# Optimization experiments

Hardware: AMD Instinct MI355X
Metric: run time of the kernel (lower is better)

The kernel has to match this reference:

```python
import jax, jax.numpy as jnp
import numpy as np

N_NODES = 50000
N_EDGES = 600000
NUM_FEATURES = 128
HIDDEN = 128
NUM_CLASSES = 64
NUM_GRAPHS = 128


def setup_inputs() -> dict:
    key = jax.random.key(0)
    ks = jax.random.split(key, 10)
    x = jax.random.normal(ks[0], (N_NODES, NUM_FEATURES), dtype=jnp.float32)
    edge_index = jax.random.randint(ks[1], (2, N_EDGES), 0, N_NODES, dtype=jnp.int64)
    batch = jnp.sort(jax.random.randint(ks[2], (N_NODES,), 0, NUM_GRAPHS, dtype=jnp.int64))
    def glorot(k, fan_in, fan_out):
        s = jnp.sqrt(6.0 / (fan_in + fan_out)).astype(jnp.float32)
        return jax.random.uniform(k, (fan_in, fan_out), jnp.float32, -s, s)
    W0 = glorot(ks[3], NUM_FEATURES, HIDDEN)
    b0 = jnp.zeros((HIDDEN,), jnp.float32)
    W1 = glorot(ks[4], HIDDEN, HIDDEN)
    b1 = jnp.zeros((HIDDEN,), jnp.float32)
    W2 = glorot(ks[5], HIDDEN, NUM_CLASSES)
    b2 = jnp.zeros((NUM_CLASSES,), jnp.float32)
    return {"x": x, "edge_index": edge_index, "batch": batch,
            "W0": W0, "b0": b0, "W1": W1, "b1": b1, "W2": W2, "b2": b2}


def _gcn_norm(edge_index, n_nodes):
    # add self loops, compute symmetric normalization coeffs (PyG GCNConv)
    loops = jnp.arange(n_nodes, dtype=edge_index.dtype)
    src = jnp.concatenate([edge_index[0], loops])
    dst = jnp.concatenate([edge_index[1], loops])
    deg = jax.ops.segment_sum(jnp.ones_like(dst, dtype=jnp.float32), dst,
                              num_segments=n_nodes)
    dinv = jnp.where(deg > 0, jax.lax.rsqrt(deg), 0.0)
    norm = dinv[src] * dinv[dst]  # [E + N]
    return src, dst, norm


def _gcn_conv(x, src, dst, norm, W, b, n_nodes):
    h = x @ W                                   # [N, out]
    msg = h[src] * norm[:, None]                # gather + scale per edge
    out = jax.ops.segment_sum(msg, dst, num_segments=n_nodes)  # scatter-add
    return out + b


def reference(x, edge_index, batch, W0, b0, W1, b1, W2, b2):
    n = x.shape[0]
    src, dst, norm = _gcn_norm(edge_index, n)
    h = jax.nn.relu(_gcn_conv(x, src, dst, norm, W0, b0, n))
    # F.dropout(training=self.training) is identity in eval mode
    h = jax.nn.relu(_gcn_conv(h, src, dst, norm, W1, b1, n))
    h = _gcn_conv(h, src, dst, norm, W2, b2, n)
    # global_mean_pool over batch vector
    sums = jax.ops.segment_sum(h, batch, num_segments=NUM_GRAPHS)
    cnts = jax.ops.segment_sum(jnp.ones((n,), jnp.float32), batch,
                               num_segments=NUM_GRAPHS)
    pooled = sums / jnp.maximum(cnts, 1.0)[:, None]  # [G, num_classes]
    return jax.nn.softmax(pooled, axis=1)
```

## Files before the change

kernel.cpp:

```cpp
#include <hip/hip_runtime.h>
#include <cstdint>
#include <cstddef>

typedef unsigned int uint32;


__global__ __launch_bounds__(256) void count_kernel(const int* __restrict__ dst,
                                                    int* __restrict__ counts, int e) {
  int i = blockIdx.x * 256 + threadIdx.x;
  if (i < e) atomicAdd(&counts[dst[i]], 1);
}

__global__ __launch_bounds__(256) void dinv_kernel(const int* __restrict__ counts,
                                                   float* __restrict__ dinv, int n) {
  int i = blockIdx.x * 256 + threadIdx.x;
  if (i < n) dinv[i] = rsqrtf((float)(counts[i] + 1));
}

__global__ __launch_bounds__(256) void scan1_kernel(const int* __restrict__ counts,
                                                    int* __restrict__ bsum, int n) {
  __shared__ int lds[256];
  int tid = threadIdx.x;
  int i = blockIdx.x * 256 + tid;
  lds[tid] = (i < n) ? counts[i] : 0;
  __syncthreads();
  for (int off = 128; off > 0; off >>= 1) {
    if (tid < off) lds[tid] += lds[tid + off];
    __syncthreads();
  }
  if (tid == 0) bsum[blockIdx.x] = lds[0];
}

__global__ __launch_bounds__(256) void scan2_kernel(int* __restrict__ bsum, int nb) {
  __shared__ int lds[256];
  int tid = threadIdx.x;
  int v = (tid < nb) ? bsum[tid] : 0;
  lds[tid] = v;
  __syncthreads();
  for (int off = 1; off < 256; off <<= 1) {
    int t = (tid >= off) ? lds[tid - off] : 0;
    __syncthreads();
    lds[tid] += t;
    __syncthreads();
  }
  if (tid < nb) bsum[tid] = lds[tid] - v;
}

__global__ __launch_bounds__(256) void scan3_kernel(const int* __restrict__ counts,
                                                    const int* __restrict__ bsum,
                                                    int* __restrict__ offsets, int n) {
  __shared__ int lds[256];
  int tid = threadIdx.x;
  int i = blockIdx.x * 256 + tid;
  int v = (i < n) ? counts[i] : 0;
  lds[tid] = v;
  __syncthreads();
  for (int off = 1; off < 256; off <<= 1) {
    int t = (tid >= off) ? lds[tid - off] : 0;
    __syncthreads();
    lds[tid] += t;
    __syncthreads();
  }
  if (i < n) offsets[i] = bsum[blockIdx.x] + lds[tid] - v;
}

__global__ __launch_bounds__(256) void scatter_kernel(const int* __restrict__ src,
                                                      const int* __restrict__ dst,
                                                      const float* __restrict__ dinv,
                                                      int* __restrict__ offsets,
                                                      int2* __restrict__ csr_sw, int e) {
  int i = blockIdx.x * 256 + threadIdx.x;
  if (i < e) {
    int d = dst[i], s = src[i];
    int pos = atomicAdd(&offsets[d], 1);
    csr_sw[pos] = make_int2(s, __float_as_int(dinv[s] * dinv[d]));
  }
}

__device__ __forceinline__ uint32 bf16pair(float a, float b) {
  uint32 ua = __float_as_uint(a);
  uint32 ub = __float_as_uint(b);
  ua += 0x7fffu + ((ua >> 16) & 1u);
  ub += 0x7fffu + ((ub >> 16) & 1u);
  return (ua >> 16) | (ub & 0xffff0000u);
}


template <int BM, int BN>
__global__ __launch_bounds__(256) void gemm_kernel(const float* __restrict__ X,
                                                   const float* __restrict__ W,
                                                   uint32* __restrict__ T, int M) {
  constexpr int K = 128;
  static_assert(BM * BN == 4096, "4x4 tile x 256 threads");
  __shared__ float xs[K][BM];
  __shared__ float ws[K][BN];

  int tid = threadIdx.x;
  int row0 = blockIdx.x * BM;

  {
    constexpr int TPR = 256 / BM;
    int r = tid / TPR;
    int lw = tid % TPR;
    int grow = row0 + r;
    if (grow >= M) grow = M - 1;
    const float* xp = &X[(size_t)grow * K];
#pragma unroll
    for (int u = 0; u < K / (4 * TPR); ++u) {
      int k = (lw + u * TPR) * 4;
      float4 v = *(const float4*)&xp[k];
      xs[k + 0][r] = v.x;
      xs[k + 1][r] = v.y;
      xs[k + 2][r] = v.z;
      xs[k + 3][r] = v.w;
    }
  }
  {
    const float4* wsrc = (const float4*)W;
    float4* wdst = (float4*)&ws[0][0];
#pragma unroll
    for (int u = 0; u < (K * BN) / 1024; ++u)
      wdst[tid + u * 256] = wsrc[tid + u * 256];
  }
  __syncthreads();

  int r0 = (tid % (BM / 4)) * 4;
  int c0 = (tid / (BM / 4)) * 4;
  float acc[4][4];
#pragma unroll
  for (int i = 0; i < 4; ++i)
#pragma unroll
    for (int j = 0; j < 4; ++j) acc[i][j] = 0.f;

#pragma unroll 8
  for (int k = 0; k < K; ++k) {
    float4 a = *(const float4*)&xs[k][r0];
    float4 b = *(const float4*)&ws[k][c0];
    float av[4] = {a.x, a.y, a.z, a.w};
    float bv[4] = {b.x, b.y, b.z, b.w};
#pragma unroll
    for (int i = 0; i < 4; ++i)
#pragma unroll
      for (int j = 0; j < 4; ++j) acc[i][j] += av[i] * bv[j];
  }

#pragma unroll
  for (int i = 0; i < 4; ++i) {
    int grow = row0 + r0 + i;
    if (grow < M) {
      uint2 o;
      o.x = bf16pair(acc[i][0], acc[i][1]);
      o.y = bf16pair(acc[i][2], acc[i][3]);
      *(uint2*)&T[((size_t)grow * BN + c0) >> 1] = o;
    }
  }
}


template <int F, bool RELU>
__global__ __launch_bounds__(256) void agg_kernel(const uint32* __restrict__ T,
                                                  const int2* __restrict__ csr_sw,
                                                  const int* __restrict__ offsets,
                                                  const int* __restrict__ counts,
                                                  const float* __restrict__ dinv,
                                                  const float* __restrict__ bias,
                                                  float* __restrict__ O, int n) {
  constexpr int LPN = F / 8;
  constexpr int NPB = 256 / LPN;
  constexpr int RS = F / 8;
  int tid = threadIdx.x;
  int lane = tid % LPN;
  int v = blockIdx.x * NPB + tid / LPN;
  if (v >= n) return;

  const uint4* Tv = (const uint4*)T;

#define LO(u) __uint_as_float((u) << 16)
#define HI(u) __uint_as_float((u) & 0xffff0000u)

  float dv = dinv[v];
  float sw = dv * dv;
  float a0, a1, a2, a3, a4, a5, a6, a7;
  {
    uint4 q = Tv[(size_t)v * RS + lane];
    a0 = sw * LO(q.x); a1 = sw * HI(q.x);
    a2 = sw * LO(q.y); a3 = sw * HI(q.y);
    a4 = sw * LO(q.z); a5 = sw * HI(q.z);
    a6 = sw * LO(q.w); a7 = sw * HI(q.w);
  }

  int end = offsets[v];
  int i = end - counts[v];
  for (; i + 4 <= end; i += 4) {
    int2 p0 = csr_sw[i + 0];
    int2 p1 = csr_sw[i + 1];
    int2 p2 = csr_sw[i + 2];
    int2 p3 = csr_sw[i + 3];
    uint4 u0 = Tv[(size_t)p0.x * RS + lane];
    uint4 u1 = Tv[(size_t)p1.x * RS + lane];
    uint4 u2 = Tv[(size_t)p2.x * RS + lane];
    uint4 u3 = Tv[(size_t)p3.x * RS + lane];
    float w0 = __int_as_float(p0.y), w1 = __int_as_float(p1.y);
    float w2 = __int_as_float(p2.y), w3 = __int_as_float(p3.y);
    a0 += w0 * LO(u0.x); a1 += w0 * HI(u0.x); a2 += w0 * LO(u0.y); a3 += w0 * HI(u0.y);
    a4 += w0 * LO(u0.z); a5 += w0 * HI(u0.z); a6 += w0 * LO(u0.w); a7 += w0 * HI(u0.w);
    a0 += w1 * LO(u1.x); a1 += w1 * HI(u1.x); a2 += w1 * LO(u1.y); a3 += w1 * HI(u1.y);
    a4 += w1 * LO(u1.z); a5 += w1 * HI(u1.z); a6 += w1 * LO(u1.w); a7 += w1 * HI(u1.w);
    a0 += w2 * LO(u2.x); a1 += w2 * HI(u2.x); a2 += w2 * LO(u2.y); a3 += w2 * HI(u2.y);
    a4 += w2 * LO(u2.z); a5 += w2 * HI(u2.z); a6 += w2 * LO(u2.w); a7 += w2 * HI(u2.w);
    a0 += w3 * LO(u3.x); a1 += w3 * HI(u3.x); a2 += w3 * LO(u3.y); a3 += w3 * HI(u3.y);
    a4 += w3 * LO(u3.z); a5 += w3 * HI(u3.z); a6 += w3 * LO(u3.w); a7 += w3 * HI(u3.w);
  }
  for (; i < end; ++i) {
    int2 p = csr_sw[i];
    float w = __int_as_float(p.y);
    uint4 u = Tv[(size_t)p.x * RS + lane];
    a0 += w * LO(u.x); a1 += w * HI(u.x); a2 += w * LO(u.y); a3 += w * HI(u.y);
    a4 += w * LO(u.z); a5 += w * HI(u.z); a6 += w * LO(u.w); a7 += w * HI(u.w);
  }
#undef LO
#undef HI

  int fo = lane * 8;
  float4 b0 = *(const float4*)&bias[fo];
  float4 b1 = *(const float4*)&bias[fo + 4];
  a0 += b0.x; a1 += b0.y; a2 += b0.z; a3 += b0.w;
  a4 += b1.x; a5 += b1.y; a6 += b1.z; a7 += b1.w;
  if (RELU) {
    a0 = fmaxf(a0, 0.f); a1 = fmaxf(a1, 0.f); a2 = fmaxf(a2, 0.f); a3 = fmaxf(a3, 0.f);
    a4 = fmaxf(a4, 0.f); a5 = fmaxf(a5, 0.f); a6 = fmaxf(a6, 0.f); a7 = fmaxf(a7, 0.f);
  }
  float4 o0 = {a0, a1, a2, a3};
  float4 o1 = {a4, a5, a6, a7};
  *(float4*)&O[(size_t)v * F + fo] = o0;
  *(float4*)&O[(size_t)v * F + fo + 4] = o1;
}


__global__ __launch_bounds__(256) void pool_kernel(const float* __restrict__ h3,
                                                   const int* __restrict__ batch,
                                                   float* __restrict__ pooled,
                                                   float* __restrict__ gcnt, int n) {
  constexpr int NPW = 64;
  int lane = threadIdx.x & 63;
  int wave = threadIdx.x >> 6;
  int v0 = (blockIdx.x * 4 + wave) * NPW;
  if (v0 >= n) return;
  int vend = min(v0 + NPW, n);

  float acc = 0.f;
  int cnt = 0;
  int bcur = batch[v0];
  for (int v = v0; v < vend; ++v) {
    int b = batch[v];
    if (b != bcur) {
      atomicAdd(&pooled[bcur * 64 + lane], acc);
      if (lane == 0) atomicAdd(&gcnt[bcur], (float)cnt);
      acc = 0.f; cnt = 0; bcur = b;
    }
    acc += h3[(size_t)v * 64 + lane];
    ++cnt;
  }
  atomicAdd(&pooled[bcur * 64 + lane], acc);
  if (lane == 0) atomicAdd(&gcnt[bcur], (float)cnt);
}

__global__ __launch_bounds__(64) void softmax_kernel(const float* __restrict__ pooled,
                                                     const float* __restrict__ gcnt,
                                                     float* __restrict__ out) {
  int g = blockIdx.x;
  int lane = threadIdx.x;
  float c = fmaxf(gcnt[g], 1.0f);
  float v = pooled[g * 64 + lane] / c;
  float m = v;
#pragma unroll
  for (int off = 32; off >= 1; off >>= 1) m = fmaxf(m, __shfl_xor(m, off));
  float e = expf(v - m);
  float s = e;
#pragma unroll
  for (int off = 32; off >= 1; off >>= 1) s += __shfl_xor(s, off);
  out[g * 64 + lane] = e / s;
}


extern "C" void kernel_launch(void* const* d_in, const int* in_sizes, int n_in,
                              void* d_out, int out_size, void* d_ws, size_t ws_size,
                              hipStream_t stream) {
  const float* x  = (const float*)d_in[0];
  const int* edge = (const int*)d_in[1];
  const int* batch = (const int*)d_in[2];
  const float* W0 = (const float*)d_in[3];
  const float* b0 = (const float*)d_in[4];
  const float* W1 = (const float*)d_in[5];
  const float* b1 = (const float*)d_in[6];
  const float* W2 = (const float*)d_in[7];
  const float* b2 = (const float*)d_in[8];
  float* out = (float*)d_out;

  const int N = in_sizes[2];
  const int E = in_sizes[1] / 2;
  const int* esrc = edge;
  const int* edst = edge + E;

  char* p = (char*)d_ws;
  auto alloc = [&](size_t bytes) {
    char* r = p;
    p += (bytes + 255) & ~(size_t)255;
    return r;
  };
  int*    counts  = (int*)alloc((size_t)N * 4);
  int*    offsets = (int*)alloc((size_t)N * 4);
  float*  dinv    = (float*)alloc((size_t)N * 4);
  int*    bsum    = (int*)alloc(256 * 4);
  int2*   csr_sw  = (int2*)alloc((size_t)E * 8);
  uint32* Tb      = (uint32*)alloc((size_t)N * 128 * 2);
  float*  A       = (float*)alloc((size_t)N * 128 * 4);
  float*  pooled  = (float*)alloc(128 * 64 * 4);
  float*  gcnt    = (float*)alloc(128 * 4);

  int nbN = (N + 255) / 256;
  int nbE = (E + 255) / 256;

  hipMemsetAsync(counts, 0, (size_t)N * 4, stream);
  hipMemsetAsync(pooled, 0, 128 * 64 * 4, stream);
  hipMemsetAsync(gcnt, 0, 128 * 4, stream);

  count_kernel<<<nbE, 256, 0, stream>>>(edst, counts, E);
  dinv_kernel<<<nbN, 256, 0, stream>>>(counts, dinv, N);
  scan1_kernel<<<nbN, 256, 0, stream>>>(counts, bsum, N);
  scan2_kernel<<<1, 256, 0, stream>>>(bsum, nbN);
  scan3_kernel<<<nbN, 256, 0, stream>>>(counts, bsum, offsets, N);
  scatter_kernel<<<nbE, 256, 0, stream>>>(esrc, edst, dinv, offsets, csr_sw, E);

  gemm_kernel<32, 128><<<(N + 31) / 32, 256, 0, stream>>>(x, W0, Tb, N);
  agg_kernel<128, true><<<(N + 15) / 16, 256, 0, stream>>>(Tb, csr_sw, offsets,
                                                           counts, dinv, b0, A, N);
  gemm_kernel<32, 128><<<(N + 31) / 32, 256, 0, stream>>>(A, W1, Tb, N);
  agg_kernel<128, true><<<(N + 15) / 16, 256, 0, stream>>>(Tb, csr_sw, offsets,
                                                           counts, dinv, b1, A, N);
  gemm_kernel<64, 64><<<(N + 63) / 64, 256, 0, stream>>>(A, W2, Tb, N);
  agg_kernel<64, false><<<(N + 31) / 32, 256, 0, stream>>>(Tb, csr_sw, offsets,
                                                           counts, dinv, b2, A, N);

  pool_kernel<<<(N + 255) / 256, 256, 0, stream>>>(A, batch, pooled, gcnt, N);
  softmax_kernel<<<128, 64, 0, stream>>>(pooled, gcnt, out);
}
```

Before: 335.7 us.

## Switch dense GEMMs to bf16 MFMA with swizzled LDS and pretransposed weights

Replaces the fp32 FMA GEMM with a bf16 MFMA 16x16x32 kernel. Activations are converted to bf16 while being staged into XOR-swizzled shared memory, and a new prep kernel transposes and packs the weights into bf16. The aim is to move the dense transforms onto matrix cores and shrink LDS traffic. The cost is bf16 rounding of inputs and weights, which lowers GEMM precision, plus one extra small kernel launch.

```diff
diff --git a/kernel.cpp b/kernel.cpp
--- a/kernel.cpp
+++ b/kernel.cpp
@@ -3,6 +3,9 @@
 #include <cstddef>
 
 typedef unsigned int uint32;
+typedef unsigned short uint16;
+using short8 = __attribute__((ext_vector_type(8))) short;
+using f32x4 = __attribute__((ext_vector_type(4))) float;
 
 
 __global__ __launch_bounds__(256) void count_kernel(const int* __restrict__ dst,
@@ -77,81 +80,101 @@
   }
 }
 
+__device__ __forceinline__ uint32 bf16of(float a) {
+  uint32 u = __float_as_uint(a);
+  u += 0x7fffu + ((u >> 16) & 1u);
+  return u >> 16;
+}
 __device__ __forceinline__ uint32 bf16pair(float a, float b) {
-  uint32 ua = __float_as_uint(a);
-  uint32 ub = __float_as_uint(b);
-  ua += 0x7fffu + ((ua >> 16) & 1u);
-  ub += 0x7fffu + ((ub >> 16) & 1u);
-  return (ua >> 16) | (ub & 0xffff0000u);
-}
-
-
-template <int BM, int BN>
+  return bf16of(a) | (bf16of(b) << 16);
+}
+
+__global__ __launch_bounds__(256) void wprep_kernel(const float* __restrict__ W0,
+                                                    const float* __restrict__ W1,
+                                                    const float* __restrict__ W2,
+                                                    uint32* __restrict__ Wt0,
+                                                    uint32* __restrict__ Wt1,
+                                                    uint32* __restrict__ Wt2) {
+  int b = blockIdx.x;
+  const float* W; uint32* Wt; int N; int base;
+  if (b < 32)      { W = W0; Wt = Wt0; N = 128; base = b; }
+  else if (b < 64) { W = W1; Wt = Wt1; N = 128; base = b - 32; }
+  else             { W = W2; Wt = Wt2; N = 64;  base = b - 64; }
+  int id = base * 256 + threadIdx.x;
+  int col = id % N;
+  int kp = id / N;
+  if (kp >= 64) return;
+  int k = kp * 2;
+  Wt[col * 64 + kp] = bf16pair(W[(size_t)k * N + col], W[(size_t)(k + 1) * N + col]);
+}
+
+
+template <int BN>
 __global__ __launch_bounds__(256) void gemm_kernel(const float* __restrict__ X,
-                                                   const float* __restrict__ W,
-                                                   uint32* __restrict__ T, int M) {
-  constexpr int K = 128;
-  static_assert(BM * BN == 4096, "4x4 tile x 256 threads");
-  __shared__ float xs[K][BM];
-  __shared__ float ws[K][BN];
+                                                   const uint32* __restrict__ Wt,
+                                                   uint16* __restrict__ T, int M) {
+  constexpr int K = 128, BM = 64;
+  constexpr int NT = BN / 16;
+  __shared__ alignas(16) uint16 xs[BM * K];
+  __shared__ alignas(16) uint16 wsT[BN * K];
 
   int tid = threadIdx.x;
   int row0 = blockIdx.x * BM;
 
   {
-    constexpr int TPR = 256 / BM;
-    int r = tid / TPR;
-    int lw = tid % TPR;
+    int r = tid >> 2, k0 = (tid & 3) * 32;
     int grow = row0 + r;
     if (grow >= M) grow = M - 1;
     const float* xp = &X[(size_t)grow * K];
 #pragma unroll
-    for (int u = 0; u < K / (4 * TPR); ++u) {
-      int k = (lw + u * TPR) * 4;
+    for (int u = 0; u < 8; ++u) {
+      int k = k0 + u * 4;
       float4 v = *(const float4*)&xp[k];
-      xs[k + 0][r] = v.x;
-      xs[k + 1][r] = v.y;
-      xs[k + 2][r] = v.z;
-      xs[k + 3][r] = v.w;
+      uint2 pk = make_uint2(bf16pair(v.x, v.y), bf16pair(v.z, v.w));
+      int byte = (r * 256 + k * 2) ^ ((r & 7) << 4);
+      *(uint2*)((char*)xs + byte) = pk;
     }
   }
   {
-    const float4* wsrc = (const float4*)W;
-    float4* wdst = (float4*)&ws[0][0];
-#pragma unroll
-    for (int u = 0; u < (K * BN) / 1024; ++u)
-      wdst[tid + u * 256] = wsrc[tid + u * 256];
+#pragma unroll
+    for (int u = 0; u < NT; ++u) {
+      int idx = tid + u * 256;
+      int col = idx >> 4;
+      int kb = (idx & 15) << 4;
+      uint4 v = *(const uint4*)((const char*)Wt + col * 256 + kb);
+      int byte = (col * 256 + kb) ^ ((col & 7) << 4);
+      *(uint4*)((char*)wsT + byte) = v;
+    }
   }
   __syncthreads();
 
-  int r0 = (tid % (BM / 4)) * 4;
-  int c0 = (tid / (BM / 4)) * 4;
-  float acc[4][4];
-#pragma unroll
-  for (int i = 0; i < 4; ++i)
-#pragma unroll
-    for (int j = 0; j < 4; ++j) acc[i][j] = 0.f;
-
-#pragma unroll 8
-  for (int k = 0; k < K; ++k) {
-    float4 a = *(const float4*)&xs[k][r0];
-    float4 b = *(const float4*)&ws[k][c0];
-    float av[4] = {a.x, a.y, a.z, a.w};
-    float bv[4] = {b.x, b.y, b.z, b.w};
-#pragma unroll
-    for (int i = 0; i < 4; ++i)
-#pragma unroll
-      for (int j = 0; j < 4; ++j) acc[i][j] += av[i] * bv[j];
-  }
-
-#pragma unroll
-  for (int i = 0; i < 4; ++i) {
-    int grow = row0 + r0 + i;
-    if (grow < M) {
-      uint2 o;
-      o.x = bf16pair(acc[i][0], acc[i][1]);
-      o.y = bf16pair(acc[i][2], acc[i][3]);
-      *(uint2*)&T[((size_t)grow * BN + c0) >> 1] = o;
+  int w = tid >> 6, l = tid & 63;
+  int lrow = l & 15, lk = l >> 4;
+
+  f32x4 acc[NT];
+#pragma unroll
+  for (int n = 0; n < NT; ++n) acc[n] = {0.f, 0.f, 0.f, 0.f};
+
+#pragma unroll
+  for (int c = 0; c < 4; ++c) {
+    int ak = c * 32 + lk * 8;
+    int ar = w * 16 + lrow;
+    short8 afrag = *(const short8*)((const char*)xs + ((ar * 256 + ak * 2) ^ ((ar & 7) << 4)));
+#pragma unroll
+    for (int n = 0; n < NT; ++n) {
+      int bc = n * 16 + lrow;
+      short8 bfrag = *(const short8*)((const char*)wsT + ((bc * 256 + ak * 2) ^ ((bc & 7) << 4)));
+      acc[n] = __builtin_amdgcn_mfma_f32_16x16x32_bf16(afrag, bfrag, acc[n], 0, 0, 0);
+    }
+  }
+
+#pragma unroll
+  for (int n = 0; n < NT; ++n) {
+#pragma unroll
+    for (int r = 0; r < 4; ++r) {
+      int grow = row0 + w * 16 + lk * 4 + r;
+      if (grow < M)
+        T[(size_t)grow * BN + n * 16 + lrow] = (uint16)bf16of(acc[n][r]);
     }
   }
 }
@@ -313,8 +336,11 @@
   float*  dinv    = (float*)alloc((size_t)N * 4);
   int*    bsum    = (int*)alloc(256 * 4);
   int2*   csr_sw  = (int2*)alloc((size_t)E * 8);
-  uint32* Tb      = (uint32*)alloc((size_t)N * 128 * 2);
+  uint16* Tb      = (uint16*)alloc((size_t)N * 128 * 2);
   float*  A       = (float*)alloc((size_t)N * 128 * 4);
+  uint32* Wt0     = (uint32*)alloc(128 * 64 * 4);
+  uint32* Wt1     = (uint32*)alloc(128 * 64 * 4);
+  uint32* Wt2     = (uint32*)alloc(64 * 64 * 4);
   float*  pooled  = (float*)alloc(128 * 64 * 4);
   float*  gcnt    = (float*)alloc(128 * 4);
 
@@ -331,16 +357,19 @@
   scan2_kernel<<<1, 256, 0, stream>>>(bsum, nbN);
   scan3_kernel<<<nbN, 256, 0, stream>>>(counts, bsum, offsets, N);
   scatter_kernel<<<nbE, 256, 0, stream>>>(esrc, edst, dinv, offsets, csr_sw, E);
-
-  gemm_kernel<32, 128><<<(N + 31) / 32, 256, 0, stream>>>(x, W0, Tb, N);
-  agg_kernel<128, true><<<(N + 15) / 16, 256, 0, stream>>>(Tb, csr_sw, offsets,
-                                                           counts, dinv, b0, A, N);
-  gemm_kernel<32, 128><<<(N + 31) / 32, 256, 0, stream>>>(A, W1, Tb, N);
-  agg_kernel<128, true><<<(N + 15) / 16, 256, 0, stream>>>(Tb, csr_sw, offsets,
-                                                           counts, dinv, b1, A, N);
-  gemm_kernel<64, 64><<<(N + 63) / 64, 256, 0, stream>>>(A, W2, Tb, N);
-  agg_kernel<64, false><<<(N + 31) / 32, 256, 0, stream>>>(Tb, csr_sw, offsets,
-                                                           counts, dinv, b2, A, N);
+  wprep_kernel<<<80, 256, 0, stream>>>(W0, W1, W2, Wt0, Wt1, Wt2);
+
+  int nbG = (N + 63) / 64;
+
+  gemm_kernel<128><<<nbG, 256, 0, stream>>>(x, Wt0, Tb, N);
+  agg_kernel<128, true><<<(N + 15) / 16, 256, 0, stream>>>((const uint32*)Tb, csr_sw,
+                                                           offsets, counts, dinv, b0, A, N);
+  gemm_kernel<128><<<nbG, 256, 0, stream>>>(A, Wt1, Tb, N);
+  agg_kernel<128, true><<<(N + 15) / 16, 256, 0, stream>>>((const uint32*)Tb, csr_sw,
+                                                           offsets, counts, dinv, b1, A, N);
+  gemm_kernel<64><<<nbG, 256, 0, stream>>>(A, Wt2, Tb, N);
+  agg_kernel<64, false><<<(N + 31) / 32, 256, 0, stream>>>((const uint32*)Tb, csr_sw,
+                                                           offsets, counts, dinv, b2, A, N);
 
   pool_kernel<<<(N + 255) / 256, 256, 0, stream>>>(A, batch, pooled, gcnt, N);
   softmax_kernel<<<128, 64, 0, stream>>>(pooled, gcnt, out);
```

Result: faster. 283.4 us (-15.6%).
